# Kernel tuning notes

Measured on AMD Instinct MI355X. Metric: run time of the kernel, lower is better.

## Reference

```python
import math
import jax, jax.numpy as jnp
import numpy as np

D_MODEL = 1024
N_HEADS = 16
D_K = 64


def setup_inputs() -> dict:
    key = jax.random.key(0)
    ks = jax.random.split(key, 12)
    N, T = 4, 2048
    hd = N_HEADS * D_K
    s_in = 1.0 / math.sqrt(D_MODEL)
    s_hd = 1.0 / math.sqrt(hd)
    return {
        "x_k": jax.random.normal(ks[0], (N, T, D_MODEL), jnp.float32),
        "x_v": jax.random.normal(ks[1], (N, T, D_MODEL), jnp.float32),
        "x_q": jax.random.normal(ks[2], (N, T, D_MODEL), jnp.float32),
        "mask": jnp.ones((N, T), jnp.int32),
        "Wk": jax.random.normal(ks[3], (D_MODEL, hd), jnp.float32) * s_in,
        "bk": jax.random.normal(ks[4], (hd,), jnp.float32) * s_in,
        "Wv": jax.random.normal(ks[5], (D_MODEL, hd), jnp.float32) * s_in,
        "bv": jax.random.normal(ks[6], (hd,), jnp.float32) * s_in,
        "Wq": jax.random.normal(ks[7], (D_MODEL, hd), jnp.float32) * s_in,
        "bq": jax.random.normal(ks[8], (hd,), jnp.float32) * s_in,
        "Wf": jax.random.normal(ks[9], (hd, D_MODEL), jnp.float32) * s_hd,
        "bf": jax.random.normal(ks[10], (D_MODEL,), jnp.float32) * s_hd,
    }


def _split_heads(x):  # [N,T,H*D] -> [N,H,T,D]
    n, t, _ = x.shape
    return x.reshape(n, t, N_HEADS, D_K).transpose(0, 2, 1, 3)


def reference(x_k, x_v, x_q, mask, Wk, bk, Wv, bv, Wq, bq, Wf, bf):
    k = _split_heads(x_k @ Wk + bk)  # projected but (faithfully) unused in scores
    v = _split_heads(x_v @ Wv + bv)
    q = _split_heads(x_q @ Wq + bq)
    # NOTE: original code computes scores from q and v (not k) — reproduced faithfully.
    scores = jnp.einsum('nhid,nhjd->nhij', q, v) / math.sqrt(D_K)
    scores = jnp.where(mask[:, None, None, :] == 0, -jnp.inf, scores)
    weights = jax.nn.softmax(scores, axis=-1)
    A = jnp.einsum('nhij,nhjd->nhid', weights, v)  # [N,H,T,D]
    n, h, t, d = A.shape
    A = A.transpose(0, 2, 1, 3).reshape(n, t, h * d)
    return A @ Wf + bf
```

## Files before the change

kernel.cpp:

```cpp
#include <hip/hip_runtime.h>
#include <cstdint>
#include <type_traits>

typedef unsigned short u16;
typedef __attribute__((ext_vector_type(8))) short short8;
typedef __attribute__((ext_vector_type(8))) __fp16 half8;
typedef __attribute__((ext_vector_type(2))) __fp16 half2v;
typedef __attribute__((ext_vector_type(4))) float f32x4;

#define DMODEL 1024
#define TSEQ   2048
#define NHEADS 16
#define DKH    64
#define NBATCH 4
#define MROWS  (NBATCH * TSEQ)
#define QSCALE 0.18033688011f

__device__ __forceinline__ float b2f(u16 u) {
  union { unsigned int u; float f; } c; c.u = ((unsigned int)u) << 16; return c.f;
}
__device__ __forceinline__ u16 f2b(float f) {
  union { float f; unsigned int u; } c; c.f = f;
  unsigned int u = c.u;
  return (u16)((u + 0x7fffu + ((u >> 16) & 1u)) >> 16);
}
__device__ __forceinline__ half2v pkrtz(float a, float b) {
  return __builtin_amdgcn_cvt_pkrtz(a, b);
}
__device__ __forceinline__ unsigned h2u(half2v h) {
  unsigned u; __builtin_memcpy(&u, &h, 4); return u;
}
__device__ __forceinline__ u16 f2h(float f) {
  half2v h = pkrtz(f, 0.f);
  u16 u; __builtin_memcpy(&u, &h, 2); return u;
}

__device__ __forceinline__ void gl_lds16(const u16* g, u16* l) {
  __builtin_amdgcn_global_load_lds((const __attribute__((address_space(1))) void*)g,
                                   (__attribute__((address_space(3))) void*)l, 16, 0, 0);
}

__global__ void cvt_bf16(const float* __restrict__ in, u16* __restrict__ out) {
  int i = blockIdx.x * 256 + threadIdx.x;
  const float4* p = (const float4*)in + (long long)i * 2;
  float4 a = p[0], b = p[1];
  union { u16 s[8]; uint4 v; } pk;
  pk.s[0] = f2b(a.x); pk.s[1] = f2b(a.y); pk.s[2] = f2b(a.z); pk.s[3] = f2b(a.w);
  pk.s[4] = f2b(b.x); pk.s[5] = f2b(b.y); pk.s[6] = f2b(b.z); pk.s[7] = f2b(b.w);
  ((uint4*)out)[i] = pk.v;
}

template <bool F16>
__global__ void transpose_cvt(const float* __restrict__ in, u16* __restrict__ out) {
  __shared__ float t[32][33];
  int bx = blockIdx.x * 32, by = blockIdx.y * 32;
  int tx = threadIdx.x, ty = threadIdx.y;
  #pragma unroll
  for (int i = ty; i < 32; i += 8)
    t[i][tx] = in[(by + i) * DMODEL + bx + tx];
  __syncthreads();
  #pragma unroll
  for (int i = ty; i < 32; i += 8)
    out[(bx + i) * DMODEL + by + tx] = F16 ? f2h(t[tx][i]) : f2b(t[tx][i]);
}

__global__ void transpose_v(const u16* __restrict__ Vb, u16* __restrict__ VbT) {
  __shared__ u16 tl[64 * 66];
  int tb = blockIdx.x, h = blockIdx.y, nb = blockIdx.z;
  int tx = threadIdx.x, ty = threadIdx.y;
  long long src = (long long)(nb * TSEQ + tb * 64) * DMODEL + h * DKH;
  #pragma unroll
  for (int r = ty; r < 64; r += 4)
    tl[r * 66 + tx] = Vb[src + (long long)r * DMODEL + tx];
  __syncthreads();
  long long dst = (long long)((nb * NHEADS + h) * DKH) * TSEQ + tb * 64;
  #pragma unroll
  for (int r = ty; r < 64; r += 4)
    VbT[dst + (long long)r * TSEQ + tx] = f2h(b2f(tl[tx * 66 + r]));
}

template <bool F16, typename CT>
__device__ __forceinline__ void gemm_core(
    u16* As, u16* Bs,
    const u16* __restrict__ A, const u16* __restrict__ Bt,
    const float* __restrict__ bias, CT* __restrict__ C,
    const int bm, const int bn, const float osc) {
  const int tid  = threadIdx.x;
  const int wv   = tid >> 6, lane = tid & 63;
  const int wm   = wv >> 1, wn = wv & 1;
  const int l15  = lane & 15, quad = lane >> 4;
  const int srow = lane >> 3, gch = (lane & 7) ^ srow;

  f32x4 acc[4][4];
  #pragma unroll
  for (int i = 0; i < 4; ++i)
    #pragma unroll
    for (int j = 0; j < 4; ++j)
      acc[i][j] = (f32x4){0.f, 0.f, 0.f, 0.f};

  const u16* Ag = A  + (long long)(bm * 128) * DMODEL;
  const u16* Bg = Bt + (long long)(bn * 128) * DMODEL;

  for (int k0 = 0; k0 < DMODEL; k0 += 64) {
    __syncthreads();
    #pragma unroll
    for (int j = 0; j < 4; ++j) {
      int rb = wv * 32 + j * 8;
      gl_lds16(Ag + (long long)(rb + srow) * DMODEL + k0 + gch * 8, As + rb * 64);
      gl_lds16(Bg + (long long)(rb + srow) * DMODEL + k0 + gch * 8, Bs + rb * 64);
    }
    __syncthreads();
    #pragma unroll
    for (int ks = 0; ks < 2; ++ks) {
      #pragma unroll
      for (int mi = 0; mi < 4; ++mi) {
        int ra = wm * 64 + mi * 16 + l15;
        const u16* pa = As + ra * 64 + (((ks * 4 + quad) ^ (ra & 7)) * 8);
        #pragma unroll
        for (int ni = 0; ni < 4; ++ni) {
          int rb = wn * 64 + ni * 16 + l15;
          const u16* pb = Bs + rb * 64 + (((ks * 4 + quad) ^ (rb & 7)) * 8);
          if constexpr (F16)
            acc[mi][ni] = __builtin_amdgcn_mfma_f32_16x16x32_f16(
                *(const half8*)pa, *(const half8*)pb, acc[mi][ni], 0, 0, 0);
          else
            acc[mi][ni] = __builtin_amdgcn_mfma_f32_16x16x32_bf16(
                *(const short8*)pa, *(const short8*)pb, acc[mi][ni], 0, 0, 0);
        }
      }
    }
  }

  #pragma unroll
  for (int ni = 0; ni < 4; ++ni) {
    int col = bn * 128 + wn * 64 + ni * 16 + l15;
    float bvf = bias[col];
    #pragma unroll
    for (int mi = 0; mi < 4; ++mi) {
      int row0 = bm * 128 + wm * 64 + mi * 16 + quad * 4;
      #pragma unroll
      for (int r = 0; r < 4; ++r) {
        float val = (acc[mi][ni][r] + bvf) * osc;
        long long idx = (long long)(row0 + r) * DMODEL + col;
        if constexpr (std::is_same_v<CT, float>) C[idx] = val;
        else                                     C[idx] = f2b(val);
      }
    }
  }
}

__global__ __launch_bounds__(256, 4)
void gemm_qv(const u16* __restrict__ Xq, const u16* __restrict__ Xv,
             const u16* __restrict__ WqT, const u16* __restrict__ WvT,
             const float* __restrict__ bq, const float* __restrict__ bv,
             u16* __restrict__ Qb, u16* __restrict__ Vb) {
  __shared__ u16 As[128 * 64];
  __shared__ u16 Bs[128 * 64];
  const bool isq = (blockIdx.z == 0);
  gemm_core<false, u16>(As, Bs, isq ? Xq : Xv, isq ? WqT : WvT,
                        isq ? bq : bv, isq ? Qb : Vb,
                        blockIdx.x, blockIdx.y, isq ? QSCALE : 1.0f);
}

__global__ __launch_bounds__(256, 2)
void gemm_out(const u16* __restrict__ A, const u16* __restrict__ Bt,
              const float* __restrict__ bias, float* __restrict__ C) {
  __shared__ u16 As[128 * 64];
  __shared__ u16 Bs[128 * 64];
  gemm_core<true, float>(As, Bs, A, Bt, bias, C, blockIdx.x, blockIdx.y, 1.0f);
}

__global__ __launch_bounds__(256, 4)
void attn_kernel(const u16* __restrict__ Qb, const u16* __restrict__ Vb,
                 const u16* __restrict__ VbTh, const int* __restrict__ mask,
                 u16* __restrict__ Ab) {
  __shared__ u16 Vs[64 * 64];
  __shared__ u16 Vts[64 * 64];
  __shared__ u16 Ps[4 * 32 * 72];
  __shared__ float Msf[64];

  const int tid  = threadIdx.x;
  const int qblk = blockIdx.x, h = blockIdx.y, nb = blockIdx.z;
  const int wv   = tid >> 6, lane = tid & 63;
  const int l15  = lane & 15, quad = lane >> 4;
  const int srow = lane >> 3, gch = (lane & 7) ^ srow;

  const int q0 = qblk * 128 + wv * 32;
  const long long rowbase = (long long)nb * TSEQ;
  const long long hd = (long long)((nb * NHEADS + h) * DKH);
  u16* psb = Ps + wv * 32 * 72;

  short8 qf[2][2];
  #pragma unroll
  for (int mi = 0; mi < 2; ++mi)
    #pragma unroll
    for (int ks = 0; ks < 2; ++ks)
      qf[mi][ks] = *(const short8*)(Qb + (rowbase + q0 + mi * 16 + l15) * DMODEL
                                    + h * DKH + ks * 32 + quad * 8);

  f32x4 of[2][4];
  #pragma unroll
  for (int mi = 0; mi < 2; ++mi)
    #pragma unroll
    for (int dt = 0; dt < 4; ++dt)
      of[mi][dt] = (f32x4){0.f, 0.f, 0.f, 0.f};
  float lsum[2] = {0.f, 0.f};
  const half2v one2 = {(__fp16)1.f, (__fp16)1.f};

  for (int vb = 0; vb < TSEQ / 64; ++vb) {
    __syncthreads();
    #pragma unroll
    for (int j = 0; j < 2; ++j) {
      int rb = wv * 16 + j * 8;
      gl_lds16(Vb   + (rowbase + vb * 64 + rb + srow) * DMODEL + h * DKH + gch * 8, Vs  + rb * 64);
      gl_lds16(VbTh + (hd + rb + srow) * TSEQ + vb * 64 + gch * 8,                  Vts + rb * 64);
    }
    int mv = mask[nb * TSEQ + vb * 64 + lane];
    if (tid < 64) Msf[tid] = mv ? 0.f : -INFINITY;
    const bool slowm = __any(mv == 0);
    __syncthreads();

    f32x4 st[2][4];
    #pragma unroll
    for (int mi = 0; mi < 2; ++mi)
      #pragma unroll
      for (int tt = 0; tt < 4; ++tt)
        st[mi][tt] = (f32x4){0.f, 0.f, 0.f, 0.f};
    #pragma unroll
    for (int tt = 0; tt < 4; ++tt) {
      int r = tt * 16 + l15;
      #pragma unroll
      for (int ks = 0; ks < 2; ++ks) {
        short8 vf = *(const short8*)(Vs + r * 64 + (((ks * 4 + quad) ^ (l15 & 7)) * 8));
        #pragma unroll
        for (int mi = 0; mi < 2; ++mi)
          st[mi][tt] = __builtin_amdgcn_mfma_f32_16x16x32_bf16(vf, qf[mi][ks], st[mi][tt], 0, 0, 0);
      }
    }

    f32x4 msk[4];
    if (slowm) {
      #pragma unroll
      for (int tt = 0; tt < 4; ++tt)
        msk[tt] = *(const f32x4*)(Msf + tt * 16 + quad * 4);
    }
    #pragma unroll
    for (int mi = 0; mi < 2; ++mi) {
      #pragma unroll
      for (int tt = 0; tt < 4; ++tt) {
        float a0 = st[mi][tt][0], a1 = st[mi][tt][1];
        float a2 = st[mi][tt][2], a3 = st[mi][tt][3];
        if (slowm) { a0 += msk[tt][0]; a1 += msk[tt][1]; a2 += msk[tt][2]; a3 += msk[tt][3]; }
        float p0 = __builtin_amdgcn_exp2f(a0);
        float p1 = __builtin_amdgcn_exp2f(a1);
        float p2 = __builtin_amdgcn_exp2f(a2);
        float p3 = __builtin_amdgcn_exp2f(a3);
        half2v h01 = pkrtz(p0, p1), h23 = pkrtz(p2, p3);
#if __has_builtin(__builtin_amdgcn_fdot2)
        lsum[mi] = __builtin_amdgcn_fdot2(h01, one2, lsum[mi], false);
        lsum[mi] = __builtin_amdgcn_fdot2(h23, one2, lsum[mi], false);
#else
        lsum[mi] += (p0 + p1) + (p2 + p3);
#endif
        uint2 pk; pk.x = h2u(h01); pk.y = h2u(h23);
        *(uint2*)(psb + (mi * 16 + l15) * 72 + tt * 16 + quad * 4) = pk;
      }
    }

    #pragma unroll
    for (int kc = 0; kc < 2; ++kc) {
      half8 pf[2];
      #pragma unroll
      for (int mi = 0; mi < 2; ++mi)
        pf[mi] = *(const half8*)(psb + (mi * 16 + l15) * 72 + kc * 32 + quad * 8);
      #pragma unroll
      for (int dt = 0; dt < 4; ++dt) {
        int r = dt * 16 + l15;
        half8 vtf = *(const half8*)(Vts + r * 64 + (((kc * 4 + quad) ^ (l15 & 7)) * 8));
        #pragma unroll
        for (int mi = 0; mi < 2; ++mi)
          of[mi][dt] = __builtin_amdgcn_mfma_f32_16x16x32_f16(vtf, pf[mi], of[mi][dt], 0, 0, 0);
      }
    }
  }

  #pragma unroll
  for (int mi = 0; mi < 2; ++mi) {
    float l = lsum[mi];
    l += __shfl_xor(l, 16, 64);
    l += __shfl_xor(l, 32, 64);
    float inv = 1.0f / l;
    long long row = rowbase + q0 + mi * 16 + l15;
    #pragma unroll
    for (int dt = 0; dt < 4; ++dt) {
      uint2 o;
      o.x = h2u(pkrtz(of[mi][dt][0] * inv, of[mi][dt][1] * inv));
      o.y = h2u(pkrtz(of[mi][dt][2] * inv, of[mi][dt][3] * inv));
      *(uint2*)(Ab + row * DMODEL + h * DKH + dt * 16 + quad * 4) = o;
    }
  }
}

extern "C" void kernel_launch(void* const* d_in, const int* in_sizes, int n_in,
                              void* d_out, int out_size, void* d_ws, size_t ws_size,
                              hipStream_t stream) {
  const float* x_v  = (const float*)d_in[1];
  const float* x_q  = (const float*)d_in[2];
  const int*   mask = (const int*)d_in[3];
  const float* Wv   = (const float*)d_in[6];
  const float* bv   = (const float*)d_in[7];
  const float* Wq   = (const float*)d_in[8];
  const float* bq   = (const float*)d_in[9];
  const float* Wf   = (const float*)d_in[10];
  const float* bfp  = (const float*)d_in[11];

  char* w = (char*)d_ws;
  u16* WqT  = (u16*)(w + 0);
  u16* WvT  = (u16*)(w + (2ll << 20));
  u16* WfT  = (u16*)(w + (4ll << 20));
  u16* Xq   = (u16*)(w + (6ll << 20));
  u16* Xv   = (u16*)(w + (22ll << 20));
  u16* Qb   = (u16*)(w + (38ll << 20));
  u16* Vb   = (u16*)(w + (54ll << 20));
  u16* VbTh = (u16*)(w + (70ll << 20));
  u16* Ab   = Xq;

  dim3 tb(32, 8), tg(32, 32);
  transpose_cvt<false><<<tg, tb, 0, stream>>>(Wq, WqT);
  transpose_cvt<false><<<tg, tb, 0, stream>>>(Wv, WvT);
  transpose_cvt<true ><<<tg, tb, 0, stream>>>(Wf, WfT);

  cvt_bf16<<<MROWS * DMODEL / 8 / 256, 256, 0, stream>>>(x_q, Xq);
  cvt_bf16<<<MROWS * DMODEL / 8 / 256, 256, 0, stream>>>(x_v, Xv);

  gemm_qv<<<dim3(MROWS / 128, DMODEL / 128, 2), 256, 0, stream>>>(
      Xq, Xv, WqT, WvT, bq, bv, Qb, Vb);

  transpose_v<<<dim3(TSEQ / 64, NHEADS, NBATCH), dim3(64, 4), 0, stream>>>(Vb, VbTh);

  attn_kernel<<<dim3(TSEQ / 128, NHEADS, NBATCH), 256, 0, stream>>>(Qb, Vb, VbTh, mask, Ab);

  gemm_out<<<dim3(MROWS / 128, DMODEL / 128), 256, 0, stream>>>(Ab, WfT, bfp, (float*)d_out);
}
```

Before: 323.4 us.

## Double attention KV tile to 128 keys and batch prep kernel launches

The attention kernel now loads 128 keys of V and V-transposed per iteration instead of 64, halving the number of block-wide barriers and loop iterations. The transposed-V tile layout becomes 128 wide with a new XOR swizzle, and the mask is staged for 128 keys. Launch bounds drop from 4 to 3 blocks per CU to make room for the larger LDS footprint. The three weight-transpose launches are merged into one grid using blockIdx.z, and so are the two input-conversion launches, to cut launch overhead.

New measurement: 340.3 us. +5.2%, slower.

```diff
diff --git a/kernel.cpp b/kernel.cpp
--- a/kernel.cpp
+++ b/kernel.cpp
@@ -40,7 +40,10 @@
                                    (__attribute__((address_space(3))) void*)l, 16, 0, 0);
 }
 
-__global__ void cvt_bf16(const float* __restrict__ in, u16* __restrict__ out) {
+__global__ void cvt_bf16(const float* __restrict__ in0, u16* __restrict__ out0,
+                         const float* __restrict__ in1, u16* __restrict__ out1) {
+  const float* in = blockIdx.z ? in1 : in0;
+  u16* out = blockIdx.z ? out1 : out0;
   int i = blockIdx.x * 256 + threadIdx.x;
   const float4* p = (const float4*)in + (long long)i * 2;
   float4 a = p[0], b = p[1];
@@ -50,8 +53,12 @@
   ((uint4*)out)[i] = pk.v;
 }
 
-template <bool F16>
-__global__ void transpose_cvt(const float* __restrict__ in, u16* __restrict__ out) {
+__global__ void transpose_cvt(const float* __restrict__ w0, u16* __restrict__ o0,
+                              const float* __restrict__ w1, u16* __restrict__ o1,
+                              const float* __restrict__ w2, u16* __restrict__ o2) {
+  const int z = blockIdx.z;
+  const float* in = (z == 0) ? w0 : (z == 1) ? w1 : w2;
+  u16* out = (z == 0) ? o0 : (z == 1) ? o1 : o2;
   __shared__ float t[32][33];
   int bx = blockIdx.x * 32, by = blockIdx.y * 32;
   int tx = threadIdx.x, ty = threadIdx.y;
@@ -61,7 +68,7 @@
   __syncthreads();
   #pragma unroll
   for (int i = ty; i < 32; i += 8)
-    out[(bx + i) * DMODEL + by + tx] = F16 ? f2h(t[tx][i]) : f2b(t[tx][i]);
+    out[(bx + i) * DMODEL + by + tx] = (z == 2) ? f2h(t[tx][i]) : f2b(t[tx][i]);
 }
 
 __global__ void transpose_v(const u16* __restrict__ Vb, u16* __restrict__ VbT) {
@@ -170,14 +177,14 @@
   gemm_core<true, float>(As, Bs, A, Bt, bias, C, blockIdx.x, blockIdx.y, 1.0f);
 }
 
-__global__ __launch_bounds__(256, 4)
+__global__ __launch_bounds__(256, 3)
 void attn_kernel(const u16* __restrict__ Qb, const u16* __restrict__ Vb,
                  const u16* __restrict__ VbTh, const int* __restrict__ mask,
                  u16* __restrict__ Ab) {
-  __shared__ u16 Vs[64 * 64];
-  __shared__ u16 Vts[64 * 64];
+  __shared__ u16 Vs[128 * 64];
+  __shared__ u16 Vts[64 * 128];
   __shared__ u16 Ps[4 * 32 * 72];
-  __shared__ float Msf[64];
+  __shared__ float Msf[128];
 
   const int tid  = threadIdx.x;
   const int qblk = blockIdx.x, h = blockIdx.y, nb = blockIdx.z;
@@ -207,79 +214,91 @@
   float lsum[2] = {0.f, 0.f};
   const half2v one2 = {(__fp16)1.f, (__fp16)1.f};
 
-  for (int vb = 0; vb < TSEQ / 64; ++vb) {
+  for (int vb = 0; vb < TSEQ / 128; ++vb) {
     __syncthreads();
     #pragma unroll
-    for (int j = 0; j < 2; ++j) {
-      int rb = wv * 16 + j * 8;
-      gl_lds16(Vb   + (rowbase + vb * 64 + rb + srow) * DMODEL + h * DKH + gch * 8, Vs  + rb * 64);
-      gl_lds16(VbTh + (hd + rb + srow) * TSEQ + vb * 64 + gch * 8,                  Vts + rb * 64);
-    }
-    int mv = mask[nb * TSEQ + vb * 64 + lane];
-    if (tid < 64) Msf[tid] = mv ? 0.f : -INFINITY;
-    const bool slowm = __any(mv == 0);
+    for (int j = 0; j < 4; ++j) {
+      int rb = wv * 32 + j * 8;
+      gl_lds16(Vb + (rowbase + vb * 128 + rb + srow) * DMODEL + h * DKH + gch * 8,
+               Vs + rb * 64);
+    }
+    #pragma unroll
+    for (int j = 0; j < 4; ++j) {
+      int rb = wv * 16 + j * 4;
+      int r  = rb + (lane >> 4);
+      int g  = (lane & 15) ^ (r & 7);
+      gl_lds16(VbTh + (hd + r) * TSEQ + vb * 128 + g * 8, Vts + rb * 128);
+    }
+    int mv0 = mask[nb * TSEQ + vb * 128 + lane];
+    int mv1 = mask[nb * TSEQ + vb * 128 + 64 + lane];
+    if (tid < 128) Msf[tid] = mask[nb * TSEQ + vb * 128 + tid] ? 0.f : -INFINITY;
+    const bool slowm = __any((mv0 == 0) || (mv1 == 0));
     __syncthreads();
 
-    f32x4 st[2][4];
-    #pragma unroll
-    for (int mi = 0; mi < 2; ++mi)
-      #pragma unroll
-      for (int tt = 0; tt < 4; ++tt)
-        st[mi][tt] = (f32x4){0.f, 0.f, 0.f, 0.f};
-    #pragma unroll
-    for (int tt = 0; tt < 4; ++tt) {
-      int r = tt * 16 + l15;
-      #pragma unroll
-      for (int ks = 0; ks < 2; ++ks) {
-        short8 vf = *(const short8*)(Vs + r * 64 + (((ks * 4 + quad) ^ (l15 & 7)) * 8));
+    #pragma unroll
+    for (int th = 0; th < 2; ++th) {
+      f32x4 st[2][4];
+      #pragma unroll
+      for (int mi = 0; mi < 2; ++mi)
+        #pragma unroll
+        for (int tt = 0; tt < 4; ++tt)
+          st[mi][tt] = (f32x4){0.f, 0.f, 0.f, 0.f};
+      #pragma unroll
+      for (int tt = 0; tt < 4; ++tt) {
+        int r = th * 64 + tt * 16 + l15;
+        #pragma unroll
+        for (int ks = 0; ks < 2; ++ks) {
+          short8 vf = *(const short8*)(Vs + r * 64 + (((ks * 4 + quad) ^ (l15 & 7)) * 8));
+          #pragma unroll
+          for (int mi = 0; mi < 2; ++mi)
+            st[mi][tt] = __builtin_amdgcn_mfma_f32_16x16x32_bf16(vf, qf[mi][ks], st[mi][tt], 0, 0, 0);
+        }
+      }
+
+      f32x4 msk[4];
+      if (slowm) {
+        #pragma unroll
+        for (int tt = 0; tt < 4; ++tt)
+          msk[tt] = *(const f32x4*)(Msf + th * 64 + tt * 16 + quad * 4);
+      }
+      #pragma unroll
+      for (int mi = 0; mi < 2; ++mi) {
+        #pragma unroll
+        for (int tt = 0; tt < 4; ++tt) {
+          float a0 = st[mi][tt][0], a1 = st[mi][tt][1];
+          float a2 = st[mi][tt][2], a3 = st[mi][tt][3];
+          if (slowm) { a0 += msk[tt][0]; a1 += msk[tt][1]; a2 += msk[tt][2]; a3 += msk[tt][3]; }
+          float p0 = __builtin_amdgcn_exp2f(a0);
+          float p1 = __builtin_amdgcn_exp2f(a1);
+          float p2 = __builtin_amdgcn_exp2f(a2);
+          float p3 = __builtin_amdgcn_exp2f(a3);
+          half2v h01 = pkrtz(p0, p1), h23 = pkrtz(p2, p3);
+#if __has_builtin(__builtin_amdgcn_fdot2)
+          lsum[mi] = __builtin_amdgcn_fdot2(h01, one2, lsum[mi], false);
+          lsum[mi] = __builtin_amdgcn_fdot2(h23, one2, lsum[mi], false);
+#else
+          lsum[mi] += (p0 + p1) + (p2 + p3);
+#endif
+          uint2 pk; pk.x = h2u(h01); pk.y = h2u(h23);
+          *(uint2*)(psb + (mi * 16 + l15) * 72 + tt * 16 + quad * 4) = pk;
+        }
+      }
+
+      #pragma unroll
+      for (int kc = 0; kc < 2; ++kc) {
+        half8 pf[2];
         #pragma unroll
         for (int mi = 0; mi < 2; ++mi)
-          st[mi][tt] = __builtin_amdgcn_mfma_f32_16x16x32_bf16(vf, qf[mi][ks], st[mi][tt], 0, 0, 0);
-      }
-    }
-
-    f32x4 msk[4];
-    if (slowm) {
-      #pragma unroll
-      for (int tt = 0; tt < 4; ++tt)
-        msk[tt] = *(const f32x4*)(Msf + tt * 16 + quad * 4);
-    }
-    #pragma unroll
-    for (int mi = 0; mi < 2; ++mi) {
-      #pragma unroll
-      for (int tt = 0; tt < 4; ++tt) {
-        float a0 = st[mi][tt][0], a1 = st[mi][tt][1];
-        float a2 = st[mi][tt][2], a3 = st[mi][tt][3];
-        if (slowm) { a0 += msk[tt][0]; a1 += msk[tt][1]; a2 += msk[tt][2]; a3 += msk[tt][3]; }
-        float p0 = __builtin_amdgcn_exp2f(a0);
-        float p1 = __builtin_amdgcn_exp2f(a1);
-        float p2 = __builtin_amdgcn_exp2f(a2);
-        float p3 = __builtin_amdgcn_exp2f(a3);
-        half2v h01 = pkrtz(p0, p1), h23 = pkrtz(p2, p3);
-#if __has_builtin(__builtin_amdgcn_fdot2)
-        lsum[mi] = __builtin_amdgcn_fdot2(h01, one2, lsum[mi], false);
-        lsum[mi] = __builtin_amdgcn_fdot2(h23, one2, lsum[mi], false);
-#else
-        lsum[mi] += (p0 + p1) + (p2 + p3);
-#endif
-        uint2 pk; pk.x = h2u(h01); pk.y = h2u(h23);
-        *(uint2*)(psb + (mi * 16 + l15) * 72 + tt * 16 + quad * 4) = pk;
-      }
-    }
-
-    #pragma unroll
-    for (int kc = 0; kc < 2; ++kc) {
-      half8 pf[2];
-      #pragma unroll
-      for (int mi = 0; mi < 2; ++mi)
-        pf[mi] = *(const half8*)(psb + (mi * 16 + l15) * 72 + kc * 32 + quad * 8);
-      #pragma unroll
-      for (int dt = 0; dt < 4; ++dt) {
-        int r = dt * 16 + l15;
-        half8 vtf = *(const half8*)(Vts + r * 64 + (((kc * 4 + quad) ^ (l15 & 7)) * 8));
-        #pragma unroll
-        for (int mi = 0; mi < 2; ++mi)
-          of[mi][dt] = __builtin_amdgcn_mfma_f32_16x16x32_f16(vtf, pf[mi], of[mi][dt], 0, 0, 0);
+          pf[mi] = *(const half8*)(psb + (mi * 16 + l15) * 72 + kc * 32 + quad * 8);
+        #pragma unroll
+        for (int dt = 0; dt < 4; ++dt) {
+          int r = dt * 16 + l15;
+          half8 vtf = *(const half8*)(Vts + r * 128 +
+                        (((th * 8 + kc * 4 + quad) ^ (l15 & 7)) * 8));
+          #pragma unroll
+          for (int mi = 0; mi < 2; ++mi)
+            of[mi][dt] = __builtin_amdgcn_mfma_f32_16x16x32_f16(vtf, pf[mi], of[mi][dt], 0, 0, 0);
+        }
       }
     }
   }
@@ -325,13 +344,9 @@
   u16* VbTh = (u16*)(w + (70ll << 20));
   u16* Ab   = Xq;
 
-  dim3 tb(32, 8), tg(32, 32);
-  transpose_cvt<false><<<tg, tb, 0, stream>>>(Wq, WqT);
-  transpose_cvt<false><<<tg, tb, 0, stream>>>(Wv, WvT);
-  transpose_cvt<true ><<<tg, tb, 0, stream>>>(Wf, WfT);
-
-  cvt_bf16<<<MROWS * DMODEL / 8 / 256, 256, 0, stream>>>(x_q, Xq);
-  cvt_bf16<<<MROWS * DMODEL / 8 / 256, 256, 0, stream>>>(x_v, Xv);
+  transpose_cvt<<<dim3(32, 32, 3), dim3(32, 8), 0, stream>>>(Wq, WqT, Wv, WvT, Wf, WfT);
+
+  cvt_bf16<<<dim3(MROWS * DMODEL / 8 / 256, 1, 2), 256, 0, stream>>>(x_q, Xq, x_v, Xv);
 
   gemm_qv<<<dim3(MROWS / 128, DMODEL / 128, 2), 256, 0, stream>>>(
       Xq, Xv, WqT, WvT, bq, bv, Qb, Vb);
```

## Enlarge GEMM M-tile to 256, preload fragments, and fuse prep kernels

Applied to the files above, without the earlier changes.

The five conversion and transpose launches are merged into one prep kernel that dispatches on block index. Both GEMMs move from a 128x128 to a 256x128 block tile, with each wave computing 128x64 outputs. Each k-step now loads A and B fragments into registers once before running the MFMA loop, which improves operand reuse and cuts launch overhead. In exchange, accumulator register pressure and LDS per block roughly double, qv occupancy drops from 4 to 2 blocks, and grids are halved (gemm_out gets 256 blocks).

Result: slower. 331.2 us (+2.4%).

```diff
diff --git a/kernel.cpp b/kernel.cpp
--- a/kernel.cpp
+++ b/kernel.cpp
@@ -40,28 +40,38 @@
                                    (__attribute__((address_space(3))) void*)l, 16, 0, 0);
 }
 
-__global__ void cvt_bf16(const float* __restrict__ in, u16* __restrict__ out) {
-  int i = blockIdx.x * 256 + threadIdx.x;
-  const float4* p = (const float4*)in + (long long)i * 2;
-  float4 a = p[0], b = p[1];
-  union { u16 s[8]; uint4 v; } pk;
-  pk.s[0] = f2b(a.x); pk.s[1] = f2b(a.y); pk.s[2] = f2b(a.z); pk.s[3] = f2b(a.w);
-  pk.s[4] = f2b(b.x); pk.s[5] = f2b(b.y); pk.s[6] = f2b(b.z); pk.s[7] = f2b(b.w);
-  ((uint4*)out)[i] = pk.v;
-}
-
-template <bool F16>
-__global__ void transpose_cvt(const float* __restrict__ in, u16* __restrict__ out) {
-  __shared__ float t[32][33];
-  int bx = blockIdx.x * 32, by = blockIdx.y * 32;
-  int tx = threadIdx.x, ty = threadIdx.y;
+__global__ void prep(const float* __restrict__ xq, u16* __restrict__ Xq,
+                     const float* __restrict__ xv, u16* __restrict__ Xv,
+                     const float* __restrict__ Wq, u16* __restrict__ WqT,
+                     const float* __restrict__ Wv, u16* __restrict__ WvT,
+                     const float* __restrict__ Wf, u16* __restrict__ WfT) {
+  const int bid = blockIdx.x, tid = threadIdx.x;
+  if (bid < 8192) {
+    const float* in = (bid < 4096) ? xq : xv;
+    u16* out = (bid < 4096) ? Xq : Xv;
+    int i = (bid & 4095) * 256 + tid;
+    const float4* p = (const float4*)in + (long long)i * 2;
+    float4 a = p[0], b = p[1];
+    union { u16 s[8]; uint4 v; } pk;
+    pk.s[0] = f2b(a.x); pk.s[1] = f2b(a.y); pk.s[2] = f2b(a.z); pk.s[3] = f2b(a.w);
+    pk.s[4] = f2b(b.x); pk.s[5] = f2b(b.y); pk.s[6] = f2b(b.z); pk.s[7] = f2b(b.w);
+    ((uint4*)out)[i] = pk.v;
+    return;
+  }
+  const int t = bid - 8192;
+  const int z = t >> 10, r = t & 1023;
+  const float* in = (z == 0) ? Wq : (z == 1) ? Wv : Wf;
+  u16* out = (z == 0) ? WqT : (z == 1) ? WvT : WfT;
+  __shared__ float tl[32][33];
+  int bx = (r & 31) * 32, by = (r >> 5) * 32;
+  int tx = tid & 31, ty = tid >> 5;
   #pragma unroll
   for (int i = ty; i < 32; i += 8)
-    t[i][tx] = in[(by + i) * DMODEL + bx + tx];
+    tl[i][tx] = in[(by + i) * DMODEL + bx + tx];
   __syncthreads();
   #pragma unroll
   for (int i = ty; i < 32; i += 8)
-    out[(bx + i) * DMODEL + by + tx] = F16 ? f2h(t[tx][i]) : f2b(t[tx][i]);
+    out[(bx + i) * DMODEL + by + tx] = (z == 2) ? f2h(tl[tx][i]) : f2b(tl[tx][i]);
 }
 
 __global__ void transpose_v(const u16* __restrict__ Vb, u16* __restrict__ VbT) {
@@ -91,43 +101,53 @@
   const int l15  = lane & 15, quad = lane >> 4;
   const int srow = lane >> 3, gch = (lane & 7) ^ srow;
 
-  f32x4 acc[4][4];
-  #pragma unroll
-  for (int i = 0; i < 4; ++i)
+  f32x4 acc[8][4];
+  #pragma unroll
+  for (int i = 0; i < 8; ++i)
     #pragma unroll
     for (int j = 0; j < 4; ++j)
       acc[i][j] = (f32x4){0.f, 0.f, 0.f, 0.f};
 
-  const u16* Ag = A  + (long long)(bm * 128) * DMODEL;
+  const u16* Ag = A  + (long long)(bm * 256) * DMODEL;
   const u16* Bg = Bt + (long long)(bn * 128) * DMODEL;
 
   for (int k0 = 0; k0 < DMODEL; k0 += 64) {
     __syncthreads();
     #pragma unroll
+    for (int j = 0; j < 8; ++j) {
+      int rb = wv * 64 + j * 8;
+      gl_lds16(Ag + (long long)(rb + srow) * DMODEL + k0 + gch * 8, As + rb * 64);
+    }
+    #pragma unroll
     for (int j = 0; j < 4; ++j) {
       int rb = wv * 32 + j * 8;
-      gl_lds16(Ag + (long long)(rb + srow) * DMODEL + k0 + gch * 8, As + rb * 64);
       gl_lds16(Bg + (long long)(rb + srow) * DMODEL + k0 + gch * 8, Bs + rb * 64);
     }
     __syncthreads();
     #pragma unroll
     for (int ks = 0; ks < 2; ++ks) {
-      #pragma unroll
-      for (int mi = 0; mi < 4; ++mi) {
-        int ra = wm * 64 + mi * 16 + l15;
-        const u16* pa = As + ra * 64 + (((ks * 4 + quad) ^ (ra & 7)) * 8);
+      short8 af[8], bf_[4];
+      #pragma unroll
+      for (int mi = 0; mi < 8; ++mi) {
+        int ra = wm * 128 + mi * 16 + l15;
+        af[mi] = *(const short8*)(As + ra * 64 + (((ks * 4 + quad) ^ (ra & 7)) * 8));
+      }
+      #pragma unroll
+      for (int ni = 0; ni < 4; ++ni) {
+        int rb = wn * 64 + ni * 16 + l15;
+        bf_[ni] = *(const short8*)(Bs + rb * 64 + (((ks * 4 + quad) ^ (rb & 7)) * 8));
+      }
+      #pragma unroll
+      for (int mi = 0; mi < 8; ++mi)
         #pragma unroll
         for (int ni = 0; ni < 4; ++ni) {
-          int rb = wn * 64 + ni * 16 + l15;
-          const u16* pb = Bs + rb * 64 + (((ks * 4 + quad) ^ (rb & 7)) * 8);
           if constexpr (F16)
             acc[mi][ni] = __builtin_amdgcn_mfma_f32_16x16x32_f16(
-                *(const half8*)pa, *(const half8*)pb, acc[mi][ni], 0, 0, 0);
+                *(const half8*)&af[mi], *(const half8*)&bf_[ni], acc[mi][ni], 0, 0, 0);
           else
             acc[mi][ni] = __builtin_amdgcn_mfma_f32_16x16x32_bf16(
-                *(const short8*)pa, *(const short8*)pb, acc[mi][ni], 0, 0, 0);
+                af[mi], bf_[ni], acc[mi][ni], 0, 0, 0);
         }
-      }
     }
   }
 
@@ -136,8 +156,8 @@
     int col = bn * 128 + wn * 64 + ni * 16 + l15;
     float bvf = bias[col];
     #pragma unroll
-    for (int mi = 0; mi < 4; ++mi) {
-      int row0 = bm * 128 + wm * 64 + mi * 16 + quad * 4;
+    for (int mi = 0; mi < 8; ++mi) {
+      int row0 = bm * 256 + wm * 128 + mi * 16 + quad * 4;
       #pragma unroll
       for (int r = 0; r < 4; ++r) {
         float val = (acc[mi][ni][r] + bvf) * osc;
@@ -149,12 +169,12 @@
   }
 }
 
-__global__ __launch_bounds__(256, 4)
+__global__ __launch_bounds__(256, 2)
 void gemm_qv(const u16* __restrict__ Xq, const u16* __restrict__ Xv,
              const u16* __restrict__ WqT, const u16* __restrict__ WvT,
              const float* __restrict__ bq, const float* __restrict__ bv,
              u16* __restrict__ Qb, u16* __restrict__ Vb) {
-  __shared__ u16 As[128 * 64];
+  __shared__ u16 As[256 * 64];
   __shared__ u16 Bs[128 * 64];
   const bool isq = (blockIdx.z == 0);
   gemm_core<false, u16>(As, Bs, isq ? Xq : Xv, isq ? WqT : WvT,
@@ -165,7 +185,7 @@
 __global__ __launch_bounds__(256, 2)
 void gemm_out(const u16* __restrict__ A, const u16* __restrict__ Bt,
               const float* __restrict__ bias, float* __restrict__ C) {
-  __shared__ u16 As[128 * 64];
+  __shared__ u16 As[256 * 64];
   __shared__ u16 Bs[128 * 64];
   gemm_core<true, float>(As, Bs, A, Bt, bias, C, blockIdx.x, blockIdx.y, 1.0f);
 }
@@ -325,20 +345,14 @@
   u16* VbTh = (u16*)(w + (70ll << 20));
   u16* Ab   = Xq;
 
-  dim3 tb(32, 8), tg(32, 32);
-  transpose_cvt<false><<<tg, tb, 0, stream>>>(Wq, WqT);
-  transpose_cvt<false><<<tg, tb, 0, stream>>>(Wv, WvT);
-  transpose_cvt<true ><<<tg, tb, 0, stream>>>(Wf, WfT);
-
-  cvt_bf16<<<MROWS * DMODEL / 8 / 256, 256, 0, stream>>>(x_q, Xq);
-  cvt_bf16<<<MROWS * DMODEL / 8 / 256, 256, 0, stream>>>(x_v, Xv);
-
-  gemm_qv<<<dim3(MROWS / 128, DMODEL / 128, 2), 256, 0, stream>>>(
+  prep<<<11264, 256, 0, stream>>>(x_q, Xq, x_v, Xv, Wq, WqT, Wv, WvT, Wf, WfT);
+
+  gemm_qv<<<dim3(MROWS / 256, DMODEL / 128, 2), 256, 0, stream>>>(
       Xq, Xv, WqT, WvT, bq, bv, Qb, Vb);
 
   transpose_v<<<dim3(TSEQ / 64, NHEADS, NBATCH), dim3(64, 4), 0, stream>>>(Vb, VbTh);
 
   attn_kernel<<<dim3(TSEQ / 128, NHEADS, NBATCH), 256, 0, stream>>>(Qb, Vb, VbTh, mask, Ab);
 
-  gemm_out<<<dim3(MROWS / 128, DMODEL / 128), 256, 0, stream>>>(Ab, WfT, bfp, (float*)d_out);
-}
+  gemm_out<<<dim3(MROWS / 256, DMODEL / 128), 256, 0, stream>>>(Ab, WfT, bfp, (float*)d_out);
+}
```
